# Performance work log

Hardware: AMD Instinct MI355X
Metric: run time of the kernel (lower is better)

Reference implementation:

```python
import jax, jax.numpy as jnp
import numpy as np

N, E, L = 50000, 800000, 200000
IN_FEATS, HID = 256, 128
EPS = 1e-5


def setup_inputs() -> dict:
    key = jax.random.key(0)
    ks = jax.random.split(key, 32)
    def lin(k, fan_in, fan_out):
        s = 1.0 / np.sqrt(fan_in)
        return jax.random.uniform(k, (fan_out, fan_in), jnp.float32, -s, s)
    inp = {
        "x": jax.random.normal(ks[0], (N, IN_FEATS), jnp.float32),
        "edge_index": jax.random.randint(ks[1], (2, E), 0, N, jnp.int32),
        "edge_label_index": jax.random.randint(ks[2], (2, L), 0, N, jnp.int32),
        # SAGEConv layers: lin_l (on aggregated neighbors, with bias), lin_r (root, no bias)
        "w1l": lin(ks[3], IN_FEATS, HID), "b1l": jnp.zeros((HID,), jnp.float32), "w1r": lin(ks[4], IN_FEATS, HID),
        "w2l": lin(ks[5], HID, HID), "b2l": jnp.zeros((HID,), jnp.float32), "w2r": lin(ks[6], HID, HID),
        "w3l": lin(ks[7], HID, HID), "b3l": jnp.zeros((HID,), jnp.float32), "w3r": lin(ks[8], HID, HID),
        # BatchNorm (eval mode: running stats)
        "bn1_g": jnp.ones((HID,), jnp.float32), "bn1_b": jnp.zeros((HID,), jnp.float32),
        "bn1_m": 0.1 * jax.random.normal(ks[9], (HID,), jnp.float32),
        "bn1_v": jax.random.uniform(ks[10], (HID,), jnp.float32, 0.5, 1.5),
        "bn2_g": jnp.ones((HID,), jnp.float32), "bn2_b": jnp.zeros((HID,), jnp.float32),
        "bn2_m": 0.1 * jax.random.normal(ks[11], (HID,), jnp.float32),
        "bn2_v": jax.random.uniform(ks[12], (HID,), jnp.float32, 0.5, 1.5),
        # Decoder MLP
        "dw1": lin(ks[13], 2 * HID, HID), "db1": jnp.zeros((HID,), jnp.float32),
        "dw2": lin(ks[14], HID, 1), "db2": jnp.zeros((1,), jnp.float32),
    }
    return inp


def _sage_conv(x, src, dst, wl, bl, wr):
    # mean-aggregate neighbor features at dst, then lin_l(agg) + lin_r(x)
    n = x.shape[0]
    agg = jax.ops.segment_sum(x[src], dst, num_segments=n)
    cnt = jax.ops.segment_sum(jnp.ones_like(dst, dtype=x.dtype), dst, num_segments=n)
    mean = agg / jnp.maximum(cnt, 1.0)[:, None]
    return mean @ wl.T + bl + x @ wr.T


def _bn_eval(h, g, b, m, v):
    return (h - m) * (g * jax.lax.rsqrt(v + EPS)) + b


def reference(x, edge_index, edge_label_index,
              w1l, b1l, w1r, w2l, b2l, w2r, w3l, b3l, w3r,
              bn1_g, bn1_b, bn1_m, bn1_v, bn2_g, bn2_b, bn2_m, bn2_v,
              dw1, db1, dw2, db2):
    src, dst = edge_index[0], edge_index[1]
    h = _sage_conv(x, src, dst, w1l, b1l, w1r)
    h = jax.nn.relu(_bn_eval(h, bn1_g, bn1_b, bn1_m, bn1_v))
    h = _sage_conv(h, src, dst, w2l, b2l, w2r)
    h = jax.nn.relu(_bn_eval(h, bn2_g, bn2_b, bn2_m, bn2_v))
    z = _sage_conv(h, src, dst, w3l, b3l, w3r)
    # decode: gather pair embeddings, concat, MLP -> scalar per pair
    s, d = edge_label_index[0], edge_label_index[1]
    pair = jnp.concatenate([z[s], z[d]], axis=1)  # [L, 2*HID]
    hdec = jax.nn.relu(pair @ dw1.T + db1)
    return (hdec @ dw2.T + db2).reshape(-1)
```

## Files before the change

### kernel.cpp

```cpp
#include <hip/hip_runtime.h>
#include <hip/hip_fp16.h>


typedef unsigned int uint;
using f16x8 = __attribute__((ext_vector_type(8))) _Float16;
using f32x4 = __attribute__((ext_vector_type(4))) float;

__device__ inline ushort f2h(float v) { return __half_as_ushort(__float2half(v)); }

__device__ inline void fsplit(float v, ushort& hi, ushort& lo) {
    __half h = __float2half(v);
    hi = __half_as_ushort(h);
    lo = __half_as_ushort(__float2half(v - __half2float(h)));
}

__device__ inline float4 h4f(uint2 r) {
    float2 fa = __half22float2(*(const __half2*)&r.x);
    float2 fb = __half22float2(*(const __half2*)&r.y);
    return make_float4(fa.x, fa.y, fb.x, fb.y);
}

__device__ inline uint swz(uint i, uint r) {
    return (i & ~63u) | ((i ^ (r << 3)) & 56u) | (i & 7u);
}

__device__ inline void gload16(const void* g, void* l) {
    __builtin_amdgcn_global_load_lds(
        (const __attribute__((address_space(1))) unsigned int*)g,
        (__attribute__((address_space(3))) unsigned int*)l, 16, 0, 0);
}

__global__ __launch_bounds__(256) void prep_kernel(
    const float* __restrict__ x, ushort* __restrict__ A3, int totalconv, int nconv,
    const int* __restrict__ dst, int* __restrict__ cnt, int* __restrict__ rank,
    int E, int ncount,
    const float* __restrict__ w1l, const float* __restrict__ w1r,
    const float* __restrict__ w2l, const float* __restrict__ w2r,
    const float* __restrict__ w3l, const float* __restrict__ w3r,
    const float* __restrict__ dw1,
    ushort* __restrict__ WS1, ushort* __restrict__ WS2,
    ushort* __restrict__ WS3, ushort* __restrict__ WS4)
{
    const int g = blockIdx.x >> 4;
    const int r16 = blockIdx.x & 15;
    if (r16 < 12) {
        int ci = g * 12 + r16;
        if (ci >= nconv) return;
        int e = ci * 256 + threadIdx.x;
        if (e >= totalconv) return;
        uint row = e >> 6;
        uint k4 = (e & 63) << 2;
        float4 v = *(const float4*)(x + (size_t)row * 256 + k4);
        ushort4 hi, lo;
        fsplit(v.x, hi.x, lo.x); fsplit(v.y, hi.y, lo.y);
        fsplit(v.z, hi.z, lo.z); fsplit(v.w, hi.w, lo.w);
        ushort* d = A3 + (size_t)row * 512;
        *(ushort4*)(d + swz(k4, row))       = hi;
        *(ushort4*)(d + swz(k4 + 256, row)) = lo;
    } else if (r16 < 15) {
        int qi = g * 3 + (r16 - 12);
        if (qi >= ncount) return;
        int i = qi * 256 + threadIdx.x;
        if (i < E) rank[i] = atomicAdd(&cnt[dst[i]], 1);
    } else {
        int w = g;
        if (w >= 1024) return;
        uint n = w & 255;
        int which = w >> 8;
        uint k = threadIdx.x;
        const float *wa, *wb;
        uint K, lda, aoff, boff;
        ushort* WS;
        switch (which) {
            case 0:  wa = w1l; wb = w1r; K = 256; lda = 256; aoff = 0; boff = 0;   WS = WS1; break;
            case 1:  wa = w2l; wb = w2r; K = 128; lda = 128; aoff = 0; boff = 0;   WS = WS2; break;
            case 2:  wa = w3l; wb = w3r; K = 128; lda = 128; aoff = 0; boff = 0;   WS = WS3; break;
            default: wa = dw1; wb = dw1; K = 128; lda = 256; aoff = 0; boff = 128; WS = WS4; break;
        }
        if (k >= K) return;
        const float* srcr = (n < 128) ? (wa + (size_t)n * lda + aoff)
                                      : (wb + (size_t)(n - 128) * lda + boff);
        ushort* d = WS + (size_t)n * K;
        d[swz(k, n)] = f2h(srcr[k]);
    }
}

__global__ void scanA_kernel(const int* __restrict__ cnt, int* __restrict__ ptr,
                             int* __restrict__ tilesum, int n) {
    __shared__ int sd[1024];
    int t = threadIdx.x;
    int i = blockIdx.x * 1024 + t;
    int v = (i < n) ? cnt[i] : 0;
    sd[t] = v;
    __syncthreads();
    #pragma unroll
    for (int off = 1; off < 1024; off <<= 1) {
        int add = (t >= off) ? sd[t - off] : 0;
        __syncthreads();
        sd[t] += add;
        __syncthreads();
    }
    if (i < n) ptr[i] = sd[t] - v;
    if (t == 1023) tilesum[blockIdx.x] = sd[t];
}

__global__ void scanC_kernel(int* __restrict__ ptr, const int* __restrict__ tilesum,
                             int n, int ntiles) {
    int i = blockIdx.x * 256 + threadIdx.x;
    int t = i >> 10;
    int base = 0;
    for (int b = 0; b < t; ++b) base += tilesum[b];
    if (i < n) ptr[i] += base;
    if (i == 0) {
        int tot = 0;
        for (int b = 0; b < ntiles; ++b) tot += tilesum[b];
        ptr[n] = tot;
    }
}

__global__ void scatter_kernel(const int* __restrict__ src, const int* __restrict__ dst,
                               const int* __restrict__ ptr, const int* __restrict__ rank,
                               int* __restrict__ edges, int E) {
    int i = blockIdx.x * blockDim.x + threadIdx.x;
    if (i < E) edges[ptr[dst[i]] + rank[i]] = src[i];
}

template <int K, int CRF16>
__global__ __launch_bounds__(256, 2) void mm_kernel(const ushort* __restrict__ A,
                                                    const ushort* __restrict__ WS,
                                                    ushort* __restrict__ Cl,
                                                    void* __restrict__ Cr_, int M) {
    constexpr int KS = K / 64;
    __shared__ ushort At[2 * 128 * 64];
    __shared__ ushort Bt[256 * 64];
    const int t = threadIdx.x;
    const int lane = t & 63;
    const int wave = t >> 6;
    const int wm = wave >> 1, wn = wave & 1;
    const int row0 = blockIdx.x * 128;
    const int l15 = lane & 15;
    const int l4 = lane >> 4;
    const int l8 = lane >> 3;
    const int c8 = lane & 7;

    f32x4 acc[4][8] = {};

    for (int s = 0; s < KS; ++s) {
        #pragma unroll
        for (int j = 0; j < 4; ++j) {
            int jj = wave + j * 4;
            int r = jj * 8 + l8;
            const ushort* ga = A + (size_t)(row0 + r) * (2 * K) + s * 64 + c8 * 8;
            gload16(ga,     (char*)At + jj * 1024 + lane * 16);
            gload16(ga + K, (char*)At + 16384 + jj * 1024 + lane * 16);
        }
        #pragma unroll
        for (int j = 0; j < 8; ++j) {
            int jj = wave + j * 4;
            int r = jj * 8 + l8;
            gload16(WS + (size_t)r * K + s * 64 + c8 * 8,
                    (char*)Bt + jj * 1024 + lane * 16);
        }
        __syncthreads();
        #pragma unroll
        for (int kk = 0; kk < 64; kk += 32) {
            f16x8 bf[8];
            #pragma unroll
            for (int ni = 0; ni < 8; ++ni) {
                int r = wn * 128 + ni * 16 + l15;
                int off = (kk + l4 * 8) ^ ((r & 7) * 8);
                bf[ni] = *(const f16x8*)&Bt[r * 64 + off];
            }
            #pragma unroll
            for (int h = 0; h < 2; ++h) {
                f16x8 af[4];
                #pragma unroll
                for (int mi = 0; mi < 4; ++mi) {
                    int r = wm * 64 + mi * 16 + l15;
                    int off = (kk + l4 * 8) ^ ((r & 7) * 8);
                    af[mi] = *(const f16x8*)&At[h * 8192 + r * 64 + off];
                }
                #pragma unroll
                for (int mi = 0; mi < 4; ++mi)
                    #pragma unroll
                    for (int ni = 0; ni < 8; ++ni)
                        acc[mi][ni] = __builtin_amdgcn_mfma_f32_16x16x32_f16(
                            af[mi], bf[ni], acc[mi][ni], 0, 0, 0);
            }
        }
        __syncthreads();
    }
    #pragma unroll
    for (int mi = 0; mi < 4; ++mi) {
        int rbase = row0 + wm * 64 + mi * 16 + l4 * 4;
        #pragma unroll
        for (int ni = 0; ni < 8; ++ni) {
            int col = ni * 16 + l15;
            #pragma unroll
            for (int j = 0; j < 4; ++j) {
                int r = rbase + j;
                if (r < M) {
                    if (wn == 0) {
                        Cl[(size_t)r * 128 + col] = f2h(acc[mi][ni][j]);
                    } else if (CRF16) {
                        ((ushort*)Cr_)[(size_t)r * 128 + col] = f2h(acc[mi][ni][j]);
                    } else {
                        ((float*)Cr_)[(size_t)r * 128 + col] = acc[mi][ni][j];
                    }
                }
            }
        }
    }
}

__global__ __launch_bounds__(256, 4) void agg_kernel(
    const ushort* __restrict__ tl, const float* __restrict__ tr,
    const int* __restrict__ ptr, const int* __restrict__ edges,
    const float* __restrict__ bl,
    const float* __restrict__ bng, const float* __restrict__ bnb,
    const float* __restrict__ bnm, const float* __restrict__ bnv,
    int do_bn, ushort* __restrict__ h3, int n) {
    const int wave = threadIdx.x >> 6;
    const int lane = threadIdx.x & 63;
    const uint node = blockIdx.x * 4 + wave;
    if (node >= (uint)n) return;
    const int half = lane >> 5;
    const uint q4 = (lane & 31) << 2;
    const int p0 = ptr[node], p1 = ptr[node + 1];
    float4 a0 = make_float4(0.f, 0.f, 0.f, 0.f), a1 = a0, a2 = a0, a3 = a0;
    float4 a4 = a0, a5 = a0, a6 = a0, a7 = a0;
    int e = p0 + half;
    int i0 = 0, i1 = 0, i2 = 0, i3 = 0, i4 = 0, i5 = 0, i6 = 0, i7 = 0;
    bool have = (e + 14 < p1);
    if (have) {
        i0 = edges[e];      i1 = edges[e + 2];  i2 = edges[e + 4];  i3 = edges[e + 6];
        i4 = edges[e + 8];  i5 = edges[e + 10]; i6 = edges[e + 12]; i7 = edges[e + 14];
    }
    while (have) {
        int c0 = i0, c1 = i1, c2 = i2, c3 = i3, c4 = i4, c5 = i5, c6 = i6, c7 = i7;
        e += 16;
        have = (e + 14 < p1);
        if (have) {
            i0 = edges[e];      i1 = edges[e + 2];  i2 = edges[e + 4];  i3 = edges[e + 6];
            i4 = edges[e + 8];  i5 = edges[e + 10]; i6 = edges[e + 12]; i7 = edges[e + 14];
        }
        uint2 r0 = *(const uint2*)(tl + (size_t)c0 * 128 + q4);
        uint2 r1 = *(const uint2*)(tl + (size_t)c1 * 128 + q4);
        uint2 r2 = *(const uint2*)(tl + (size_t)c2 * 128 + q4);
        uint2 r3 = *(const uint2*)(tl + (size_t)c3 * 128 + q4);
        uint2 r4 = *(const uint2*)(tl + (size_t)c4 * 128 + q4);
        uint2 r5 = *(const uint2*)(tl + (size_t)c5 * 128 + q4);
        uint2 r6 = *(const uint2*)(tl + (size_t)c6 * 128 + q4);
        uint2 r7 = *(const uint2*)(tl + (size_t)c7 * 128 + q4);
        float4 v0 = h4f(r0), v1 = h4f(r1), v2 = h4f(r2), v3 = h4f(r3);
        float4 v4 = h4f(r4), v5 = h4f(r5), v6 = h4f(r6), v7 = h4f(r7);
        a0.x += v0.x; a0.y += v0.y; a0.z += v0.z; a0.w += v0.w;
        a1.x += v1.x; a1.y += v1.y; a1.z += v1.z; a1.w += v1.w;
        a2.x += v2.x; a2.y += v2.y; a2.z += v2.z; a2.w += v2.w;
        a3.x += v3.x; a3.y += v3.y; a3.z += v3.z; a3.w += v3.w;
        a4.x += v4.x; a4.y += v4.y; a4.z += v4.z; a4.w += v4.w;
        a5.x += v5.x; a5.y += v5.y; a5.z += v5.z; a5.w += v5.w;
        a6.x += v6.x; a6.y += v6.y; a6.z += v6.z; a6.w += v6.w;
        a7.x += v7.x; a7.y += v7.y; a7.z += v7.z; a7.w += v7.w;
    }
    for (; e + 2 < p1; e += 4) {
        int c0 = edges[e], c1 = edges[e + 2];
        float4 v0 = h4f(*(const uint2*)(tl + (size_t)c0 * 128 + q4));
        float4 v1 = h4f(*(const uint2*)(tl + (size_t)c1 * 128 + q4));
        a0.x += v0.x; a0.y += v0.y; a0.z += v0.z; a0.w += v0.w;
        a1.x += v1.x; a1.y += v1.y; a1.z += v1.z; a1.w += v1.w;
    }
    if (e < p1) {
        int c0 = edges[e];
        float4 v0 = h4f(*(const uint2*)(tl + (size_t)c0 * 128 + q4));
        a2.x += v0.x; a2.y += v0.y; a2.z += v0.z; a2.w += v0.w;
    }
    float4 s;
    s.x = ((a0.x + a1.x) + (a2.x + a3.x)) + ((a4.x + a5.x) + (a6.x + a7.x));
    s.y = ((a0.y + a1.y) + (a2.y + a3.y)) + ((a4.y + a5.y) + (a6.y + a7.y));
    s.z = ((a0.z + a1.z) + (a2.z + a3.z)) + ((a4.z + a5.z) + (a6.z + a7.z));
    s.w = ((a0.w + a1.w) + (a2.w + a3.w)) + ((a4.w + a5.w) + (a6.w + a7.w));
    s.x += __shfl_xor(s.x, 32);
    s.y += __shfl_xor(s.y, 32);
    s.z += __shfl_xor(s.z, 32);
    s.w += __shfl_xor(s.w, 32);
    if (half == 0) {
        float inv = 1.f / fmaxf((float)(p1 - p0), 1.f);
        float4 r = *(const float4*)(tr + (size_t)node * 128 + q4);
        float4 b = *(const float4*)(bl + q4);
        float4 val;
        val.x = fmaf(s.x, inv, b.x) + r.x;
        val.y = fmaf(s.y, inv, b.y) + r.y;
        val.z = fmaf(s.z, inv, b.z) + r.z;
        val.w = fmaf(s.w, inv, b.w) + r.w;
        if (do_bn) {
            float4 g = *(const float4*)(bng + q4);
            float4 be = *(const float4*)(bnb + q4);
            float4 m = *(const float4*)(bnm + q4);
            float4 vv = *(const float4*)(bnv + q4);
            val.x = fmaxf(fmaf(val.x - m.x, g.x * rsqrtf(vv.x + 1e-5f), be.x), 0.f);
            val.y = fmaxf(fmaf(val.y - m.y, g.y * rsqrtf(vv.y + 1e-5f), be.y), 0.f);
            val.z = fmaxf(fmaf(val.z - m.z, g.z * rsqrtf(vv.z + 1e-5f), be.z), 0.f);
            val.w = fmaxf(fmaf(val.w - m.w, g.w * rsqrtf(vv.w + 1e-5f), be.w), 0.f);
        }
        ushort4 hi, lo;
        fsplit(val.x, hi.x, lo.x); fsplit(val.y, hi.y, lo.y);
        fsplit(val.z, hi.z, lo.z); fsplit(val.w, hi.w, lo.w);
        ushort* d = h3 + (size_t)node * 256;
        *(ushort4*)(d + swz(q4, node))       = hi;
        *(ushort4*)(d + swz(q4 + 128, node)) = lo;
    }
}

__global__ __launch_bounds__(256) void decode_kernel(
    const ushort* __restrict__ u, const ushort* __restrict__ v,
    const int* __restrict__ eli, const float* __restrict__ db1,
    const float* __restrict__ dw2, const float* __restrict__ db2,
    float* __restrict__ out, int L) {
    __shared__ float sb[128], sw[128];
    if (threadIdx.x < 128) {
        sb[threadIdx.x] = db1[threadIdx.x];
        sw[threadIdx.x] = dw2[threadIdx.x];
    }
    __syncthreads();
    int p = blockIdx.x * 256 + threadIdx.x;
    if (p >= L) return;
    int s = eli[p], d = eli[L + p];
    const ushort* up = u + (size_t)s * 128;
    const ushort* vp = v + (size_t)d * 128;
    float acc = db2[0];
    #pragma unroll 8
    for (int o = 0; o < 128; o += 4) {
        float4 a = h4f(*(const uint2*)(up + o));
        float4 b = h4f(*(const uint2*)(vp + o));
        float4 bb = *(const float4*)(&sb[o]);
        float4 w = *(const float4*)(&sw[o]);
        acc += fmaxf(a.x + b.x + bb.x, 0.f) * w.x;
        acc += fmaxf(a.y + b.y + bb.y, 0.f) * w.y;
        acc += fmaxf(a.z + b.z + bb.z, 0.f) * w.z;
        acc += fmaxf(a.w + b.w + bb.w, 0.f) * w.w;
    }
    out[p] = acc;
}

extern "C" void kernel_launch(void* const* d_in, const int* in_sizes, int n_in,
                              void* d_out, int out_size, void* d_ws, size_t ws_size,
                              hipStream_t stream) {
    const float* x    = (const float*)d_in[0];
    const int*   ei   = (const int*)d_in[1];
    const int*   eli  = (const int*)d_in[2];
    const float* w1l  = (const float*)d_in[3];
    const float* b1l  = (const float*)d_in[4];
    const float* w1r  = (const float*)d_in[5];
    const float* w2l  = (const float*)d_in[6];
    const float* b2l  = (const float*)d_in[7];
    const float* w2r  = (const float*)d_in[8];
    const float* w3l  = (const float*)d_in[9];
    const float* b3l  = (const float*)d_in[10];
    const float* w3r  = (const float*)d_in[11];
    const float* bn1g = (const float*)d_in[12];
    const float* bn1b = (const float*)d_in[13];
    const float* bn1m = (const float*)d_in[14];
    const float* bn1v = (const float*)d_in[15];
    const float* bn2g = (const float*)d_in[16];
    const float* bn2b = (const float*)d_in[17];
    const float* bn2m = (const float*)d_in[18];
    const float* bn2v = (const float*)d_in[19];
    const float* dw1  = (const float*)d_in[20];
    const float* db1  = (const float*)d_in[21];
    const float* dw2  = (const float*)d_in[22];
    const float* db2  = (const float*)d_in[23];
    float* out = (float*)d_out;

    const int N = in_sizes[0] / 256;
    const int E = in_sizes[1] / 2;
    const int L = in_sizes[2] / 2;
    const int* src = ei;
    const int* dst = ei + E;
    const int ntiles = (N + 1023) >> 10;
    const int nblk = (N + 127) / 128;
    const int Npad = nblk * 128;
    const int nconv = (N * 64 + 255) / 256;
    const int ncount = (E + 255) / 256;
    int G16 = (nconv + 11) / 12;
    if ((ncount + 2) / 3 > G16) G16 = (ncount + 2) / 3;
    if (1024 > G16) G16 = 1024;

    char* wsb = (char*)d_ws;
    size_t off = 0;
    auto carve = [&](size_t bytes) -> void* {
        void* p = wsb + off;
        off += (bytes + 255) & ~(size_t)255;
        return p;
    };
    int* ptr        = (int*)carve((size_t)(N + 1) * 4);
    int* cnt        = (int*)carve((size_t)N * 4);
    int* rank       = (int*)carve((size_t)E * 4);
    int* tilesum    = (int*)carve((size_t)ntiles * 4);
    int* edges      = (int*)carve((size_t)E * 4);
    ushort* WS1     = (ushort*)carve((size_t)256 * 256 * 2);
    ushort* WS2     = (ushort*)carve((size_t)256 * 128 * 2);
    ushort* WS3     = (ushort*)carve((size_t)256 * 128 * 2);
    ushort* WS4     = (ushort*)carve((size_t)256 * 128 * 2);
    ushort* tl_h    = (ushort*)carve((size_t)N * 128 * 2);
    float* tr_c     = (float*)carve((size_t)N * 128 * 4);
    ushort* A3      = (ushort*)carve((size_t)Npad * 512 * 2);
    ushort* h3      = A3;

    hipMemsetAsync(cnt, 0, (size_t)N * 4, stream);
    prep_kernel<<<G16 * 16, 256, 0, stream>>>(
        x, A3, N * 64, nconv, dst, cnt, rank, E, ncount,
        w1l, w1r, w2l, w2r, w3l, w3r, dw1, WS1, WS2, WS3, WS4);
    scanA_kernel<<<ntiles, 1024, 0, stream>>>(cnt, ptr, tilesum, N);
    scanC_kernel<<<(N + 255) / 256, 256, 0, stream>>>(ptr, tilesum, N, ntiles);
    scatter_kernel<<<(E + 255) / 256, 256, 0, stream>>>(src, dst, ptr, rank, edges, E);

    mm_kernel<256, 0><<<nblk, 256, 0, stream>>>(A3, WS1, tl_h, tr_c, N);
    agg_kernel<<<(N + 3) / 4, 256, 0, stream>>>(tl_h, tr_c, ptr, edges, b1l,
                                                bn1g, bn1b, bn1m, bn1v, 1, h3, N);
    mm_kernel<128, 0><<<nblk, 256, 0, stream>>>(h3, WS2, tl_h, tr_c, N);
    agg_kernel<<<(N + 3) / 4, 256, 0, stream>>>(tl_h, tr_c, ptr, edges, b2l,
                                                bn2g, bn2b, bn2m, bn2v, 1, h3, N);
    mm_kernel<128, 0><<<nblk, 256, 0, stream>>>(h3, WS3, tl_h, tr_c, N);
    agg_kernel<<<(N + 3) / 4, 256, 0, stream>>>(tl_h, tr_c, ptr, edges, b3l,
                                                bn1g, bn1b, bn1m, bn1v, 0, h3, N);
    mm_kernel<128, 1><<<nblk, 256, 0, stream>>>(h3, WS4, tl_h, tr_c, N);
    decode_kernel<<<(L + 255) / 256, 256, 0, stream>>>(tl_h, (const ushort*)tr_c, eli,
                                                       db1, dw2, db2, out, L);
}
```

Before: 314.0 us.

## Fuse edge scatter into first GEMM and store fp16 root term with bias

The CSR scatter kernel is folded into the first mm_kernel launch as extra blocks beyond the GEMM tiles, so the scatter runs alongside the matmul instead of as its own launch. The root-branch output (lin_r) is now written as fp16 with the bias folded in during the GEMM epilogue, halving its memory traffic and letting agg and decode skip the separate bias loads. The risk is precision loss from storing the root term in fp16, and the extra scatter blocks compete with the GEMM for resources.

```diff
diff --git a/kernel.cpp b/kernel.cpp
--- a/kernel.cpp
+++ b/kernel.cpp
@@ -118,18 +118,21 @@
     }
 }
 
-__global__ void scatter_kernel(const int* __restrict__ src, const int* __restrict__ dst,
-                               const int* __restrict__ ptr, const int* __restrict__ rank,
-                               int* __restrict__ edges, int E) {
-    int i = blockIdx.x * blockDim.x + threadIdx.x;
-    if (i < E) edges[ptr[dst[i]] + rank[i]] = src[i];
-}
-
-template <int K, int CRF16>
-__global__ __launch_bounds__(256, 2) void mm_kernel(const ushort* __restrict__ A,
-                                                    const ushort* __restrict__ WS,
-                                                    ushort* __restrict__ Cl,
-                                                    void* __restrict__ Cr_, int M) {
+template <int K, bool FUSE>
+__global__ __launch_bounds__(256, 2) void mm_kernel(
+    const ushort* __restrict__ A, const ushort* __restrict__ WS,
+    ushort* __restrict__ Cl, ushort* __restrict__ Cr,
+    const float* __restrict__ biasL, const float* __restrict__ biasR, int M,
+    int nblk, const int* __restrict__ esrc, const int* __restrict__ edst,
+    const int* __restrict__ eptr, const int* __restrict__ erank,
+    int* __restrict__ edges, int E)
+{
+    if (FUSE && blockIdx.x >= nblk) {
+        int stride = (gridDim.x - nblk) * 256;
+        for (int i = (blockIdx.x - nblk) * 256 + threadIdx.x; i < E; i += stride)
+            edges[eptr[edst[i]] + erank[i]] = esrc[i];
+        return;
+    }
     constexpr int KS = K / 64;
     __shared__ ushort At[2 * 128 * 64];
     __shared__ ushort Bt[256 * 64];
@@ -190,33 +193,27 @@
         }
         __syncthreads();
     }
+    ushort* cbase = (wn == 0) ? Cl : Cr;
+    const float* bias = (wn == 0) ? biasL : biasR;
     #pragma unroll
     for (int mi = 0; mi < 4; ++mi) {
         int rbase = row0 + wm * 64 + mi * 16 + l4 * 4;
         #pragma unroll
         for (int ni = 0; ni < 8; ++ni) {
             int col = ni * 16 + l15;
+            float bv = bias ? bias[col] : 0.f;
             #pragma unroll
             for (int j = 0; j < 4; ++j) {
                 int r = rbase + j;
-                if (r < M) {
-                    if (wn == 0) {
-                        Cl[(size_t)r * 128 + col] = f2h(acc[mi][ni][j]);
-                    } else if (CRF16) {
-                        ((ushort*)Cr_)[(size_t)r * 128 + col] = f2h(acc[mi][ni][j]);
-                    } else {
-                        ((float*)Cr_)[(size_t)r * 128 + col] = acc[mi][ni][j];
-                    }
-                }
+                if (r < M) cbase[(size_t)r * 128 + col] = f2h(acc[mi][ni][j] + bv);
             }
         }
     }
 }
 
 __global__ __launch_bounds__(256, 4) void agg_kernel(
-    const ushort* __restrict__ tl, const float* __restrict__ tr,
+    const ushort* __restrict__ tl, const ushort* __restrict__ tr,
     const int* __restrict__ ptr, const int* __restrict__ edges,
-    const float* __restrict__ bl,
     const float* __restrict__ bng, const float* __restrict__ bnb,
     const float* __restrict__ bnm, const float* __restrict__ bnv,
     int do_bn, ushort* __restrict__ h3, int n) {
@@ -286,13 +283,12 @@
     s.w += __shfl_xor(s.w, 32);
     if (half == 0) {
         float inv = 1.f / fmaxf((float)(p1 - p0), 1.f);
-        float4 r = *(const float4*)(tr + (size_t)node * 128 + q4);
-        float4 b = *(const float4*)(bl + q4);
+        float4 r = h4f(*(const uint2*)(tr + (size_t)node * 128 + q4));
         float4 val;
-        val.x = fmaf(s.x, inv, b.x) + r.x;
-        val.y = fmaf(s.y, inv, b.y) + r.y;
-        val.z = fmaf(s.z, inv, b.z) + r.z;
-        val.w = fmaf(s.w, inv, b.w) + r.w;
+        val.x = fmaf(s.x, inv, r.x);
+        val.y = fmaf(s.y, inv, r.y);
+        val.z = fmaf(s.z, inv, r.z);
+        val.w = fmaf(s.w, inv, r.w);
         if (do_bn) {
             float4 g = *(const float4*)(bng + q4);
             float4 be = *(const float4*)(bnb + q4);
@@ -314,14 +310,10 @@
 
 __global__ __launch_bounds__(256) void decode_kernel(
     const ushort* __restrict__ u, const ushort* __restrict__ v,
-    const int* __restrict__ eli, const float* __restrict__ db1,
-    const float* __restrict__ dw2, const float* __restrict__ db2,
-    float* __restrict__ out, int L) {
-    __shared__ float sb[128], sw[128];
-    if (threadIdx.x < 128) {
-        sb[threadIdx.x] = db1[threadIdx.x];
-        sw[threadIdx.x] = dw2[threadIdx.x];
-    }
+    const int* __restrict__ eli, const float* __restrict__ dw2,
+    const float* __restrict__ db2, float* __restrict__ out, int L) {
+    __shared__ float sw[128];
+    if (threadIdx.x < 128) sw[threadIdx.x] = dw2[threadIdx.x];
     __syncthreads();
     int p = blockIdx.x * 256 + threadIdx.x;
     if (p >= L) return;
@@ -333,12 +325,11 @@
     for (int o = 0; o < 128; o += 4) {
         float4 a = h4f(*(const uint2*)(up + o));
         float4 b = h4f(*(const uint2*)(vp + o));
-        float4 bb = *(const float4*)(&sb[o]);
         float4 w = *(const float4*)(&sw[o]);
-        acc += fmaxf(a.x + b.x + bb.x, 0.f) * w.x;
-        acc += fmaxf(a.y + b.y + bb.y, 0.f) * w.y;
-        acc += fmaxf(a.z + b.z + bb.z, 0.f) * w.z;
-        acc += fmaxf(a.w + b.w + bb.w, 0.f) * w.w;
+        acc += fmaxf(a.x + b.x, 0.f) * w.x;
+        acc += fmaxf(a.y + b.y, 0.f) * w.y;
+        acc += fmaxf(a.z + b.z, 0.f) * w.z;
+        acc += fmaxf(a.w + b.w, 0.f) * w.w;
     }
     out[p] = acc;
 }
@@ -403,7 +394,7 @@
     ushort* WS3     = (ushort*)carve((size_t)256 * 128 * 2);
     ushort* WS4     = (ushort*)carve((size_t)256 * 128 * 2);
     ushort* tl_h    = (ushort*)carve((size_t)N * 128 * 2);
-    float* tr_c     = (float*)carve((size_t)N * 128 * 4);
+    ushort* tr_h    = (ushort*)carve((size_t)N * 128 * 2);
     ushort* A3      = (ushort*)carve((size_t)Npad * 512 * 2);
     ushort* h3      = A3;
 
@@ -413,18 +404,25 @@
         w1l, w1r, w2l, w2r, w3l, w3r, dw1, WS1, WS2, WS3, WS4);
     scanA_kernel<<<ntiles, 1024, 0, stream>>>(cnt, ptr, tilesum, N);
     scanC_kernel<<<(N + 255) / 256, 256, 0, stream>>>(ptr, tilesum, N, ntiles);
-    scatter_kernel<<<(E + 255) / 256, 256, 0, stream>>>(src, dst, ptr, rank, edges, E);
-
-    mm_kernel<256, 0><<<nblk, 256, 0, stream>>>(A3, WS1, tl_h, tr_c, N);
-    agg_kernel<<<(N + 3) / 4, 256, 0, stream>>>(tl_h, tr_c, ptr, edges, b1l,
+
+    mm_kernel<256, true><<<nblk + 1024, 256, 0, stream>>>(
+        A3, WS1, tl_h, tr_h, nullptr, b1l, N,
+        nblk, src, dst, ptr, rank, edges, E);
+    agg_kernel<<<(N + 3) / 4, 256, 0, stream>>>(tl_h, tr_h, ptr, edges,
                                                 bn1g, bn1b, bn1m, bn1v, 1, h3, N);
-    mm_kernel<128, 0><<<nblk, 256, 0, stream>>>(h3, WS2, tl_h, tr_c, N);
-    agg_kernel<<<(N + 3) / 4, 256, 0, stream>>>(tl_h, tr_c, ptr, edges, b2l,
+    mm_kernel<128, false><<<nblk, 256, 0, stream>>>(
+        h3, WS2, tl_h, tr_h, nullptr, b2l, N,
+        0, nullptr, nullptr, nullptr, nullptr, nullptr, 0);
+    agg_kernel<<<(N + 3) / 4, 256, 0, stream>>>(tl_h, tr_h, ptr, edges,
                                                 bn2g, bn2b, bn2m, bn2v, 1, h3, N);
-    mm_kernel<128, 0><<<nblk, 256, 0, stream>>>(h3, WS3, tl_h, tr_c, N);
-    agg_kernel<<<(N + 3) / 4, 256, 0, stream>>>(tl_h, tr_c, ptr, edges, b3l,
+    mm_kernel<128, false><<<nblk, 256, 0, stream>>>(
+        h3, WS3, tl_h, tr_h, nullptr, b3l, N,
+        0, nullptr, nullptr, nullptr, nullptr, nullptr, 0);
+    agg_kernel<<<(N + 3) / 4, 256, 0, stream>>>(tl_h, tr_h, ptr, edges,
                                                 bn1g, bn1b, bn1m, bn1v, 0, h3, N);
-    mm_kernel<128, 1><<<nblk, 256, 0, stream>>>(h3, WS4, tl_h, tr_c, N);
-    decode_kernel<<<(L + 255) / 256, 256, 0, stream>>>(tl_h, (const ushort*)tr_c, eli,
-                                                       db1, dw2, db2, out, L);
-}
+    mm_kernel<128, false><<<nblk, 256, 0, stream>>>(
+        h3, WS4, tl_h, tr_h, db1, nullptr, N,
+        0, nullptr, nullptr, nullptr, nullptr, nullptr, 0);
+    decode_kernel<<<(L + 255) / 256, 256, 0, stream>>>(tl_h, tr_h, eli,
+                                                       dw2, db2, out, L);
+}
```

New measurement: 370.9 us. 1.18x slower.
